# Performance work log

Measured on AMD Instinct MI355X. Metric: run time of the kernel, lower is better.

## Reference

```python
import jax, jax.numpy as jnp
import numpy as np

EPS_DENOM = 1e-7   # epsilon added to sigmoid-sum denominator in the torch code
EPS_NORM = 1e-5    # torch InstanceNorm1d default eps


def _fcnn(x, W1, b1, W2, b2):
    # FCNN: Linear -> ReLU -> Linear
    return jax.nn.relu(x @ W1 + b1) @ W2 + b2


def setup_inputs() -> dict:
    key = jax.random.key(0)
    N, E, D, H = 100000, 1600000, 32, 128  # nodes, edges, feature dim (c_in1=c_out2), hidden (c_out1)
    ks = jax.random.split(key, 11)
    node_features = jax.random.normal(ks[0], (N, D), jnp.float32)
    edge_features = jax.random.normal(ks[1], (E, D), jnp.float32)
    edge_index = jax.random.randint(ks[2], (2, E), 0, N, dtype=jnp.int64)
    sD = 1.0 / np.sqrt(D)
    sH = 1.0 / np.sqrt(H)
    # FCNN_one params
    W1a = jax.random.normal(ks[3], (D, H), jnp.float32) * sD
    b1a = jax.random.normal(ks[4], (H,), jnp.float32) * sD
    W2a = jax.random.normal(ks[5], (H, D), jnp.float32) * sH
    b2a = jax.random.normal(ks[6], (D,), jnp.float32) * sH
    # FCNN_two params
    W1b = jax.random.normal(ks[7], (D, H), jnp.float32) * sD
    b1b = jax.random.normal(ks[8], (H,), jnp.float32) * sD
    W2b = jax.random.normal(ks[9], (H, D), jnp.float32) * sH
    b2b = jax.random.normal(ks[10], (D,), jnp.float32) * sH
    return dict(node_features=node_features, edge_features=edge_features,
                W1a=W1a, b1a=b1a, W2a=W2a, b2a=b2a,
                W1b=W1b, b1b=b1b, W2b=W2b, b2b=b2b,
                edge_index=edge_index)


def reference(node_features, edge_features, W1a, b1a, W2a, b2a,
              W1b, b1b, W2b, b2b, edge_index):
    x = node_features                      # [N, D]
    N = x.shape[0]
    h1 = _fcnn(x, W1a, b1a, W2a, b2a)      # FCNN_one(x_i) for all nodes
    h2 = _fcnn(x, W1b, b1b, W2b, b2b)      # FCNN_two(x_j) for all nodes

    s = jax.nn.sigmoid(edge_features)      # [E, D]
    # node i gathers edges where it is src OR dst (both directions)
    seg = jnp.concatenate([edge_index[0], edge_index[1]])  # [2E] center node
    nbr = jnp.concatenate([edge_index[1], edge_index[0]])  # [2E] neighbor node
    s2 = jnp.concatenate([s, s], axis=0)                   # [2E, D]

    denom = EPS_DENOM + jax.ops.segment_sum(s2, seg, num_segments=N)  # [N, D]
    msg = (s2 / denom[seg]) * h2[nbr]                                 # [2E, D]
    agg = jax.ops.segment_sum(msg, seg, num_segments=N)               # [N, D]

    h = h1 + agg
    # InstanceNorm1d over the feature dim (no affine, biased variance); dropout is identity (eval)
    mu = jnp.mean(h, axis=-1, keepdims=True)
    var = jnp.var(h, axis=-1, keepdims=True)
    hn = (h - mu) * jax.lax.rsqrt(var + EPS_NORM)
    return x + jax.nn.relu(hn)
```

## Files before the change

### kernel.cpp

```cpp
#include <hip/hip_runtime.h>

#define EPS_DENOM 1e-7f
#define EPS_NORM  1e-5f

static constexpr int D  = 32;
static constexpr int H  = 128;
static constexpr int BK = 128;
static constexpr int CHUNK = 3072;
static constexpr int CAPMAX = 6144;

typedef _Float16 f16x8 __attribute__((ext_vector_type(8)));
typedef float    f32x4 __attribute__((ext_vector_type(4)));

__global__ __launch_bounds__(256) void fcnn_mfma_kernel(
    const float* __restrict__ x,
    const float* __restrict__ W1a, const float* __restrict__ b1a,
    const float* __restrict__ W2a, const float* __restrict__ b2a,
    const float* __restrict__ W1b, const float* __restrict__ b1b,
    const float* __restrict__ W2b, const float* __restrict__ b2b,
    float* __restrict__ h1, _Float16* __restrict__ h2h, int N)
{
    __shared__ _Float16 lds[30208];
    _Float16* xk = lds;

    const int tid = threadIdx.x;
    const int nb0 = blockIdx.x * 64;

    #pragma unroll
    for (int t = 0; t < 8; ++t) {
        int f = t * 256 + tid;
        int node = f >> 5, off = f & 31;
        int gn = nb0 + node;
        float v = (gn < N) ? x[(size_t)gn * 32 + off] : 0.0f;
        xk[node * 40 + off] = (_Float16)v;
    }
    for (int fc = 0; fc < 2; ++fc) {
        const float* W1 = fc ? W1b : W1a;
        const float* W2 = fc ? W2b : W2a;
        _Float16* w1t = lds + 2560 + fc * 5120;
        _Float16* w2t = lds + 12800 + fc * 4352;
        #pragma unroll
        for (int t = 0; t < 16; ++t) {
            int f = t * 256 + tid;
            w1t[(f & 127) * 40 + (f >> 7)] = (_Float16)W1[f];
        }
        #pragma unroll
        for (int t = 0; t < 16; ++t) {
            int f = t * 256 + tid;
            w2t[(f & 31) * 136 + (f >> 5)] = (_Float16)W2[f];
        }
    }
    __syncthreads();

    const int wid  = tid >> 6;
    const int lane = tid & 63;
    const int m    = lane & 15;
    const int g    = lane >> 4;
    _Float16* t1 = lds + 21504 + wid * 2176;

    f16x8 ax = *(const f16x8*)(xk + (wid * 16 + m) * 40 + g * 8);

    for (int fc = 0; fc < 2; ++fc) {
        const float* b1v = fc ? b1b : b1a;
        const float* b2v = fc ? b2b : b2a;
        const _Float16* w1t = lds + 2560 + fc * 5120;
        const _Float16* w2t = lds + 12800 + fc * 4352;

        for (int hb = 0; hb < 8; ++hb) {
            f16x8 bw = *(const f16x8*)(w1t + (hb * 16 + m) * 40 + g * 8);
            f32x4 c = {0.f, 0.f, 0.f, 0.f};
            c = __builtin_amdgcn_mfma_f32_16x16x32_f16(ax, bw, c, 0, 0, 0);
            float bias = b1v[hb * 16 + m];
            #pragma unroll
            for (int r = 0; r < 4; ++r) {
                float tv = fmaxf(c[r] + bias, 0.0f);
                t1[(g * 4 + r) * 136 + hb * 16 + m] = (_Float16)tv;
            }
        }

        for (int dt = 0; dt < 2; ++dt) {
            f32x4 c2 = {0.f, 0.f, 0.f, 0.f};
            #pragma unroll
            for (int kc = 0; kc < 4; ++kc) {
                f16x8 a2  = *(const f16x8*)(t1 + m * 136 + kc * 32 + g * 8);
                f16x8 b2w = *(const f16x8*)(w2t + (dt * 16 + m) * 136 + kc * 32 + g * 8);
                c2 = __builtin_amdgcn_mfma_f32_16x16x32_f16(a2, b2w, c2, 0, 0, 0);
            }
            float bias = b2v[dt * 16 + m];
            #pragma unroll
            for (int r = 0; r < 4; ++r) {
                int gn = nb0 + wid * 16 + g * 4 + r;
                if (gn < N) {
                    float val = c2[r] + bias;
                    if (fc == 0) h1[(size_t)gn * 32 + dt * 16 + m] = val;
                    else         h2h[(size_t)gn * 32 + dt * 16 + m] = (_Float16)val;
                }
            }
        }
        __syncthreads();
    }
}

__global__ __launch_bounds__(256) void sprep_kernel(
    const float* __restrict__ ef, unsigned char* __restrict__ sg8, int n4)
{
    int i = blockIdx.x * blockDim.x + threadIdx.x;
    if (i >= n4) return;
    float4 v = ((const float4*)ef)[i];
    uchar4 q;
    q.x = (unsigned char)(255.0f / (1.0f + __expf(-v.x)) + 0.5f);
    q.y = (unsigned char)(255.0f / (1.0f + __expf(-v.y)) + 0.5f);
    q.z = (unsigned char)(255.0f / (1.0f + __expf(-v.z)) + 0.5f);
    q.w = (unsigned char)(255.0f / (1.0f + __expf(-v.w)) + 0.5f);
    ((uchar4*)sg8)[i] = q;
}

__global__ __launch_bounds__(256) void bin1_kernel(
    const int* __restrict__ ei, int* __restrict__ gcursor,
    uint2* __restrict__ gadj, int E, int CAP)
{
    __shared__ uint2 recs[2 * CHUNK];
    __shared__ int cnt[1024];
    __shared__ int offs[1024];
    __shared__ int gbase[1024];
    __shared__ int partial[256];

    const int tid  = threadIdx.x;
    const int base = blockIdx.x * CHUNK;
    const int ne   = min(CHUNK, E - base);

    #pragma unroll
    for (int i = 0; i < 4; ++i) cnt[tid * 4 + i] = 0;
    __syncthreads();

    int av[CHUNK / 256], bv[CHUNK / 256];
    #pragma unroll
    for (int j = 0; j < CHUNK / 256; ++j) {
        int r = j * 256 + tid;
        if (r < ne) {
            int e = base + r;
            av[j] = ei[e]; bv[j] = ei[E + e];
            atomicAdd(&cnt[av[j] >> 7], 1);
            atomicAdd(&cnt[bv[j] >> 7], 1);
        } else av[j] = -1;
    }
    __syncthreads();

    int c0 = cnt[tid*4], c1 = cnt[tid*4+1], c2 = cnt[tid*4+2], c3 = cnt[tid*4+3];
    int psum = c0 + c1 + c2 + c3;
    partial[tid] = psum;
    __syncthreads();
    for (int off = 1; off < 256; off <<= 1) {
        int t = (tid >= off) ? partial[tid - off] : 0;
        __syncthreads();
        partial[tid] += t;
        __syncthreads();
    }
    int ex = partial[tid] - psum;
    offs[tid*4]   = ex;
    offs[tid*4+1] = ex + c0;
    offs[tid*4+2] = ex + c0 + c1;
    offs[tid*4+3] = ex + c0 + c1 + c2;
    cnt[tid*4]    = ex;
    cnt[tid*4+1]  = ex + c0;
    cnt[tid*4+2]  = ex + c0 + c1;
    cnt[tid*4+3]  = ex + c0 + c1 + c2;
    __syncthreads();

    #pragma unroll
    for (int j = 0; j < CHUNK / 256; ++j) {
        if (av[j] >= 0) {
            int e = base + j * 256 + tid;
            int a = av[j], b = bv[j];
            int pa = atomicAdd(&cnt[a >> 7], 1);
            recs[pa] = make_uint2(((unsigned)(a & 127) << 21) | (unsigned)e,
                                  ((unsigned)(a >> 7) << 17) | (unsigned)b);
            int pb = atomicAdd(&cnt[b >> 7], 1);
            recs[pb] = make_uint2(((unsigned)(b & 127) << 21) | (unsigned)e,
                                  ((unsigned)(b >> 7) << 17) | (unsigned)a);
        }
    }
    __syncthreads();

    #pragma unroll
    for (int i = 0; i < 4; ++i) {
        int bidx = tid * 4 + i;
        int c = cnt[bidx] - offs[bidx];
        if (c > 0) gbase[bidx] = atomicAdd(&gcursor[bidx], c);
    }
    __syncthreads();

    int total = 2 * ne;
    for (int i = tid; i < total; i += 256) {
        uint2 r = recs[i];
        int bidx = r.y >> 17;
        int dest = gbase[bidx] + (i - offs[bidx]);
        if (dest < CAP)
            gadj[(size_t)bidx * CAP + dest] = r;
    }
}

__global__ __launch_bounds__(256) void bin2_kernel(
    const int* __restrict__ gcursor, uint2* __restrict__ gadj,
    int* __restrict__ gstart, int* __restrict__ gdeg,
    int N, int CAP)
{
    __shared__ uint2 recs[CAPMAX];
    __shared__ int cnt[BK];
    __shared__ int sc[BK];
    __shared__ int lcur[BK];

    const int tid = threadIdx.x;
    const int bk  = blockIdx.x;
    const int count = min(gcursor[bk], CAP);
    uint2* seg = gadj + (size_t)bk * CAP;

    if (tid < BK) cnt[tid] = 0;
    for (int i = tid; i < count; i += 256) recs[i] = seg[i];
    __syncthreads();

    for (int i = tid; i < count; i += 256)
        atomicAdd(&cnt[(recs[i].x >> 21) & 127], 1);
    __syncthreads();

    int v = (tid < BK) ? cnt[tid] : 0;
    if (tid < BK) sc[tid] = v;
    __syncthreads();
    for (int off = 1; off < BK; off <<= 1) {
        int t = (tid < BK && tid >= off) ? sc[tid - off] : 0;
        __syncthreads();
        if (tid < BK) sc[tid] += t;
        __syncthreads();
    }
    if (tid < BK) {
        int excl = sc[tid] - v;
        lcur[tid] = excl;
        int gn = bk * BK + tid;
        if (gn < N) {
            gstart[gn] = bk * CAP + excl;
            gdeg[gn]   = v;
        }
    }
    __syncthreads();

    for (int i = tid; i < count; i += 256) {
        uint2 r = recs[i];
        int l = (r.x >> 21) & 127;
        int pos = atomicAdd(&lcur[l], 1);
        seg[pos] = make_uint2(r.x & 0x1FFFFFu, r.y & 0x1FFFFu);
    }
}

template <bool USE_SG>
__global__ __launch_bounds__(256) void gather_kernel(
    const float* __restrict__ x,  const unsigned char* __restrict__ sg8,
    const float* __restrict__ ef, const float* __restrict__ h1,
    const _Float16* __restrict__ h2h,
    const int* __restrict__ gstart, const int* __restrict__ gdeg,
    const uint2* __restrict__ adj2,
    float* __restrict__ out, int N)
{
    int t = blockIdx.x * blockDim.x + threadIdx.x;
    int n = t >> 5;
    int d = t & 31;
    if (n >= N) return;

    int start = gstart[n];
    int end   = start + gdeg[n];

    float s_sum = 0.0f, sh_sum = 0.0f;
    int k = start;
    for (; k + 4 <= end; k += 4) {
        uint2 r0 = adj2[k+0], r1 = adj2[k+1], r2 = adj2[k+2], r3 = adj2[k+3];
        float s0, s1, s2, s3;
        if (USE_SG) {
            s0 = (float)sg8[(size_t)r0.x * 32 + d] * (1.0f / 255.0f);
            s1 = (float)sg8[(size_t)r1.x * 32 + d] * (1.0f / 255.0f);
            s2 = (float)sg8[(size_t)r2.x * 32 + d] * (1.0f / 255.0f);
            s3 = (float)sg8[(size_t)r3.x * 32 + d] * (1.0f / 255.0f);
        } else {
            s0 = 1.0f / (1.0f + __expf(-ef[(size_t)r0.x * 32 + d]));
            s1 = 1.0f / (1.0f + __expf(-ef[(size_t)r1.x * 32 + d]));
            s2 = 1.0f / (1.0f + __expf(-ef[(size_t)r2.x * 32 + d]));
            s3 = 1.0f / (1.0f + __expf(-ef[(size_t)r3.x * 32 + d]));
        }
        float h0 = (float)h2h[(size_t)r0.y * 32 + d];
        float h1v = (float)h2h[(size_t)r1.y * 32 + d];
        float h2v = (float)h2h[(size_t)r2.y * 32 + d];
        float h3 = (float)h2h[(size_t)r3.y * 32 + d];
        s_sum += (s0 + s1) + (s2 + s3);
        sh_sum = fmaf(s0, h0, sh_sum);
        sh_sum = fmaf(s1, h1v, sh_sum);
        sh_sum = fmaf(s2, h2v, sh_sum);
        sh_sum = fmaf(s3, h3, sh_sum);
    }
    for (; k < end; ++k) {
        uint2 r = adj2[k];
        float s;
        if (USE_SG) s = (float)sg8[(size_t)r.x * 32 + d] * (1.0f / 255.0f);
        else        s = 1.0f / (1.0f + __expf(-ef[(size_t)r.x * 32 + d]));
        float hh = (float)h2h[(size_t)r.y * 32 + d];
        s_sum += s;
        sh_sum = fmaf(s, hh, sh_sum);
    }

    size_t idx = (size_t)n * 32 + d;
    float h = h1[idx] + sh_sum / (EPS_DENOM + s_sum);

    float sum = h, sq = h * h;
    #pragma unroll
    for (int off = 16; off > 0; off >>= 1) {
        sum += __shfl_xor(sum, off, 32);
        sq  += __shfl_xor(sq,  off, 32);
    }
    float mu  = sum * (1.0f / 32.0f);
    float var = fmaxf(sq * (1.0f / 32.0f) - mu * mu, 0.0f);
    float hn  = (h - mu) * rsqrtf(var + EPS_NORM);

    out[idx] = x[idx] + fmaxf(hn, 0.0f);
}

extern "C" void kernel_launch(void* const* d_in, const int* in_sizes, int n_in,
                              void* d_out, int out_size, void* d_ws, size_t ws_size,
                              hipStream_t stream)
{
    const float* x   = (const float*)d_in[0];
    const float* ef  = (const float*)d_in[1];
    const float* W1a = (const float*)d_in[2];
    const float* b1a = (const float*)d_in[3];
    const float* W2a = (const float*)d_in[4];
    const float* b2a = (const float*)d_in[5];
    const float* W1b = (const float*)d_in[6];
    const float* b1b = (const float*)d_in[7];
    const float* W2b = (const float*)d_in[8];
    const float* b2b = (const float*)d_in[9];
    const int*   ei  = (const int*)d_in[10];
    float* out = (float*)d_out;

    const int N  = in_sizes[0] / D;
    const int E  = in_sizes[1] / D;
    const int NB = (N + BK - 1) / BK;
    int CAP = (2 * E) / NB;
    CAP = CAP + CAP / 2;
    CAP = (CAP + 255) & ~255;
    if (CAP > CAPMAX) CAP = CAPMAX;

    char* p = (char*)d_ws;
    float*    h1      = (float*)p;    p += (size_t)N * 32 * 4;
    _Float16* h2h     = (_Float16*)p; p += (size_t)N * 32 * 2;
    int*      gcursor = (int*)p;      p += 1024 * 4;
    int*      gstart  = (int*)p;      p += (size_t)N * 4;
    int*      gdeg    = (int*)p;      p += (size_t)N * 4;
    p = (char*)(((uintptr_t)p + 31) & ~(uintptr_t)31);
    uint2*    gadj    = (uint2*)p;    p += (size_t)NB * CAP * 8;
    p = (char*)(((uintptr_t)p + 31) & ~(uintptr_t)31);
    unsigned char* sg8 = (unsigned char*)p;
    const bool use_sg = ((size_t)(p - (char*)d_ws) + (size_t)E * 32) <= ws_size;

    hipMemsetAsync(gcursor, 0, 1024 * 4, stream);

    fcnn_mfma_kernel<<<(N + 63) / 64, 256, 0, stream>>>(
        x, W1a, b1a, W2a, b2a, W1b, b1b, W2b, b2b, h1, h2h, N);

    if (use_sg) {
        int n4 = E * 8;
        sprep_kernel<<<(n4 + 255) / 256, 256, 0, stream>>>(ef, sg8, n4);
    }

    bin1_kernel<<<(E + CHUNK - 1) / CHUNK, 256, 0, stream>>>(ei, gcursor, gadj, E, CAP);
    bin2_kernel<<<NB, 256, 0, stream>>>(gcursor, gadj, gstart, gdeg, N, CAP);

    int gthreads = N * 32;
    if (use_sg)
        gather_kernel<true><<<(gthreads + 255) / 256, 256, 0, stream>>>(
            x, sg8, ef, h1, h2h, gstart, gdeg, gadj, out, N);
    else
        gather_kernel<false><<<(gthreads + 255) / 256, 256, 0, stream>>>(
            x, sg8, ef, h1, h2h, gstart, gdeg, gadj, out, N);
}
```

Baseline: 547.6 us.

## Fuse FCNN, sigmoid quantization and binning pass into one heterogeneous launch

Merges the FCNN MFMA kernel, the sigmoid-to-uint8 prep kernel and the first binning pass into a single kernel. Blocks are divided into stripes of 8 slots: 3 FCNN tiles, 4 grid-stride sigmoid workers and 1 binning chunk, so the independent stages overlap across CUs instead of running back to back. bin2 is also widened to 512 threads. The cost is a larger shared-memory footprint for every block, which can limit occupancy, plus some block-role imbalance.

```diff
diff --git a/kernel.cpp b/kernel.cpp
--- a/kernel.cpp
+++ b/kernel.cpp
@@ -12,195 +12,232 @@
 typedef _Float16 f16x8 __attribute__((ext_vector_type(8)));
 typedef float    f32x4 __attribute__((ext_vector_type(4)));
 
-__global__ __launch_bounds__(256) void fcnn_mfma_kernel(
+__global__ __launch_bounds__(256) void prep_kernel(
     const float* __restrict__ x,
     const float* __restrict__ W1a, const float* __restrict__ b1a,
     const float* __restrict__ W2a, const float* __restrict__ b2a,
     const float* __restrict__ W1b, const float* __restrict__ b1b,
     const float* __restrict__ W2b, const float* __restrict__ b2b,
-    float* __restrict__ h1, _Float16* __restrict__ h2h, int N)
+    float* __restrict__ h1, _Float16* __restrict__ h2h,
+    const float* __restrict__ ef, unsigned char* __restrict__ sg8,
+    const int* __restrict__ ei, int* __restrict__ gcursor,
+    uint2* __restrict__ gadj,
+    int N, int E, int CAP, int F, int B, int stripes, int n4, int do_sg)
 {
-    __shared__ _Float16 lds[30208];
-    _Float16* xk = lds;
-
-    const int tid = threadIdx.x;
-    const int nb0 = blockIdx.x * 64;
-
-    #pragma unroll
-    for (int t = 0; t < 8; ++t) {
-        int f = t * 256 + tid;
-        int node = f >> 5, off = f & 31;
-        int gn = nb0 + node;
-        float v = (gn < N) ? x[(size_t)gn * 32 + off] : 0.0f;
-        xk[node * 40 + off] = (_Float16)v;
-    }
-    for (int fc = 0; fc < 2; ++fc) {
-        const float* W1 = fc ? W1b : W1a;
-        const float* W2 = fc ? W2b : W2a;
-        _Float16* w1t = lds + 2560 + fc * 5120;
-        _Float16* w2t = lds + 12800 + fc * 4352;
+    __shared__ unsigned long long smem_u64[7808];
+
+    const int tid    = threadIdx.x;
+    const int stripe = blockIdx.x >> 3;
+    const int slot   = blockIdx.x & 7;
+
+    if (slot < 3) {
+        const int fid = stripe * 3 + slot;
+        if (fid >= F) return;
+        _Float16* lds = (_Float16*)smem_u64;
+        _Float16* xk  = lds;
+        const int nb0 = fid * 64;
+
         #pragma unroll
-        for (int t = 0; t < 16; ++t) {
+        for (int t = 0; t < 8; ++t) {
             int f = t * 256 + tid;
-            w1t[(f & 127) * 40 + (f >> 7)] = (_Float16)W1[f];
-        }
-        #pragma unroll
-        for (int t = 0; t < 16; ++t) {
-            int f = t * 256 + tid;
-            w2t[(f & 31) * 136 + (f >> 5)] = (_Float16)W2[f];
-        }
-    }
-    __syncthreads();
-
-    const int wid  = tid >> 6;
-    const int lane = tid & 63;
-    const int m    = lane & 15;
-    const int g    = lane >> 4;
-    _Float16* t1 = lds + 21504 + wid * 2176;
-
-    f16x8 ax = *(const f16x8*)(xk + (wid * 16 + m) * 40 + g * 8);
-
-    for (int fc = 0; fc < 2; ++fc) {
-        const float* b1v = fc ? b1b : b1a;
-        const float* b2v = fc ? b2b : b2a;
-        const _Float16* w1t = lds + 2560 + fc * 5120;
-        const _Float16* w2t = lds + 12800 + fc * 4352;
-
-        for (int hb = 0; hb < 8; ++hb) {
-            f16x8 bw = *(const f16x8*)(w1t + (hb * 16 + m) * 40 + g * 8);
-            f32x4 c = {0.f, 0.f, 0.f, 0.f};
-            c = __builtin_amdgcn_mfma_f32_16x16x32_f16(ax, bw, c, 0, 0, 0);
-            float bias = b1v[hb * 16 + m];
+            int node = f >> 5, off = f & 31;
+            int gn = nb0 + node;
+            float v = (gn < N) ? x[(size_t)gn * 32 + off] : 0.0f;
+            xk[node * 40 + off] = (_Float16)v;
+        }
+        for (int fc = 0; fc < 2; ++fc) {
+            const float* W1 = fc ? W1b : W1a;
+            const float* W2 = fc ? W2b : W2a;
+            _Float16* w1t = lds + 2560 + fc * 5120;
+            _Float16* w2t = lds + 12800 + fc * 4352;
             #pragma unroll
-            for (int r = 0; r < 4; ++r) {
-                float tv = fmaxf(c[r] + bias, 0.0f);
-                t1[(g * 4 + r) * 136 + hb * 16 + m] = (_Float16)tv;
+            for (int t = 0; t < 16; ++t) {
+                int f = t * 256 + tid;
+                w1t[(f & 127) * 40 + (f >> 7)] = (_Float16)W1[f];
             }
-        }
-
-        for (int dt = 0; dt < 2; ++dt) {
-            f32x4 c2 = {0.f, 0.f, 0.f, 0.f};
             #pragma unroll
-            for (int kc = 0; kc < 4; ++kc) {
-                f16x8 a2  = *(const f16x8*)(t1 + m * 136 + kc * 32 + g * 8);
-                f16x8 b2w = *(const f16x8*)(w2t + (dt * 16 + m) * 136 + kc * 32 + g * 8);
-                c2 = __builtin_amdgcn_mfma_f32_16x16x32_f16(a2, b2w, c2, 0, 0, 0);
+            for (int t = 0; t < 16; ++t) {
+                int f = t * 256 + tid;
+                w2t[(f & 31) * 136 + (f >> 5)] = (_Float16)W2[f];
             }
-            float bias = b2v[dt * 16 + m];
-            #pragma unroll
-            for (int r = 0; r < 4; ++r) {
-                int gn = nb0 + wid * 16 + g * 4 + r;
-                if (gn < N) {
-                    float val = c2[r] + bias;
-                    if (fc == 0) h1[(size_t)gn * 32 + dt * 16 + m] = val;
-                    else         h2h[(size_t)gn * 32 + dt * 16 + m] = (_Float16)val;
+        }
+        __syncthreads();
+
+        const int wid  = tid >> 6;
+        const int lane = tid & 63;
+        const int m    = lane & 15;
+        const int g    = lane >> 4;
+        _Float16* t1 = lds + 21504 + wid * 2176;
+
+        f16x8 ax = *(const f16x8*)(xk + (wid * 16 + m) * 40 + g * 8);
+
+        for (int fc = 0; fc < 2; ++fc) {
+            const float* b1v = fc ? b1b : b1a;
+            const float* b2v = fc ? b2b : b2a;
+            const _Float16* w1t = lds + 2560 + fc * 5120;
+            const _Float16* w2t = lds + 12800 + fc * 4352;
+
+            for (int hb = 0; hb < 8; ++hb) {
+                f16x8 bw = *(const f16x8*)(w1t + (hb * 16 + m) * 40 + g * 8);
+                f32x4 c = {0.f, 0.f, 0.f, 0.f};
+                c = __builtin_amdgcn_mfma_f32_16x16x32_f16(ax, bw, c, 0, 0, 0);
+                float bias = b1v[hb * 16 + m];
+                #pragma unroll
+                for (int r = 0; r < 4; ++r) {
+                    float tv = fmaxf(c[r] + bias, 0.0f);
+                    t1[(g * 4 + r) * 136 + hb * 16 + m] = (_Float16)tv;
                 }
             }
-        }
-        __syncthreads();
+
+            for (int dt = 0; dt < 2; ++dt) {
+                f32x4 c2 = {0.f, 0.f, 0.f, 0.f};
+                #pragma unroll
+                for (int kc = 0; kc < 4; ++kc) {
+                    f16x8 a2  = *(const f16x8*)(t1 + m * 136 + kc * 32 + g * 8);
+                    f16x8 b2w = *(const f16x8*)(w2t + (dt * 16 + m) * 136 + kc * 32 + g * 8);
+                    c2 = __builtin_amdgcn_mfma_f32_16x16x32_f16(a2, b2w, c2, 0, 0, 0);
+                }
+                float bias = b2v[dt * 16 + m];
+                #pragma unroll
+                for (int r = 0; r < 4; ++r) {
+                    int gn = nb0 + wid * 16 + g * 4 + r;
+                    if (gn < N) {
+                        float val = c2[r] + bias;
+                        if (fc == 0) h1[(size_t)gn * 32 + dt * 16 + m] = val;
+                        else         h2h[(size_t)gn * 32 + dt * 16 + m] = (_Float16)val;
+                    }
+                }
+            }
+            __syncthreads();
+        }
+    } else if (slot < 7) {
+        if (!do_sg) return;
+        const int sid  = stripe * 4 + (slot - 3);
+        const int nthr = stripes * 4 * 256;
+        const float4* efc = (const float4*)ef;
+        uchar4* sq = (uchar4*)sg8;
+        int i = sid * 256 + tid;
+        for (; i + 3 * nthr < n4; i += 4 * nthr) {
+            float4 v0 = efc[i];
+            float4 v1 = efc[i + nthr];
+            float4 v2 = efc[i + 2 * nthr];
+            float4 v3 = efc[i + 3 * nthr];
+            uchar4 q0, q1, q2, q3;
+            q0.x = (unsigned char)(255.0f / (1.0f + __expf(-v0.x)) + 0.5f);
+            q0.y = (unsigned char)(255.0f / (1.0f + __expf(-v0.y)) + 0.5f);
+            q0.z = (unsigned char)(255.0f / (1.0f + __expf(-v0.z)) + 0.5f);
+            q0.w = (unsigned char)(255.0f / (1.0f + __expf(-v0.w)) + 0.5f);
+            q1.x = (unsigned char)(255.0f / (1.0f + __expf(-v1.x)) + 0.5f);
+            q1.y = (unsigned char)(255.0f / (1.0f + __expf(-v1.y)) + 0.5f);
+            q1.z = (unsigned char)(255.0f / (1.0f + __expf(-v1.z)) + 0.5f);
+            q1.w = (unsigned char)(255.0f / (1.0f + __expf(-v1.w)) + 0.5f);
+            q2.x = (unsigned char)(255.0f / (1.0f + __expf(-v2.x)) + 0.5f);
+            q2.y = (unsigned char)(255.0f / (1.0f + __expf(-v2.y)) + 0.5f);
+            q2.z = (unsigned char)(255.0f / (1.0f + __expf(-v2.z)) + 0.5f);
+            q2.w = (unsigned char)(255.0f / (1.0f + __expf(-v2.w)) + 0.5f);
+            q3.x = (unsigned char)(255.0f / (1.0f + __expf(-v3.x)) + 0.5f);
+            q3.y = (unsigned char)(255.0f / (1.0f + __expf(-v3.y)) + 0.5f);
+            q3.z = (unsigned char)(255.0f / (1.0f + __expf(-v3.z)) + 0.5f);
+            q3.w = (unsigned char)(255.0f / (1.0f + __expf(-v3.w)) + 0.5f);
+            sq[i]            = q0;
+            sq[i + nthr]     = q1;
+            sq[i + 2 * nthr] = q2;
+            sq[i + 3 * nthr] = q3;
+        }
+        for (; i < n4; i += nthr) {
+            float4 v = efc[i];
+            uchar4 q;
+            q.x = (unsigned char)(255.0f / (1.0f + __expf(-v.x)) + 0.5f);
+            q.y = (unsigned char)(255.0f / (1.0f + __expf(-v.y)) + 0.5f);
+            q.z = (unsigned char)(255.0f / (1.0f + __expf(-v.z)) + 0.5f);
+            q.w = (unsigned char)(255.0f / (1.0f + __expf(-v.w)) + 0.5f);
+            sq[i] = q;
+        }
+    } else {
+        const int bid = stripe;
+        if (bid >= B) return;
+        uint2* recs  = (uint2*)smem_u64;
+        int* cnt     = (int*)((char*)smem_u64 + 49152);
+        int* offs    = (int*)((char*)smem_u64 + 53248);
+        int* gbase   = (int*)((char*)smem_u64 + 57344);
+        int* partial = (int*)((char*)smem_u64 + 61440);
+
+        const int base = bid * CHUNK;
+        const int ne   = min(CHUNK, E - base);
+
+        #pragma unroll
+        for (int i = 0; i < 4; ++i) cnt[tid * 4 + i] = 0;
+        __syncthreads();
+
+        int av[CHUNK / 256], bv[CHUNK / 256];
+        #pragma unroll
+        for (int j = 0; j < CHUNK / 256; ++j) {
+            int r = j * 256 + tid;
+            if (r < ne) {
+                int e = base + r;
+                av[j] = ei[e]; bv[j] = ei[E + e];
+                atomicAdd(&cnt[av[j] >> 7], 1);
+                atomicAdd(&cnt[bv[j] >> 7], 1);
+            } else av[j] = -1;
+        }
+        __syncthreads();
+
+        int c0 = cnt[tid*4], c1 = cnt[tid*4+1], c2 = cnt[tid*4+2], c3 = cnt[tid*4+3];
+        int psum = c0 + c1 + c2 + c3;
+        partial[tid] = psum;
+        __syncthreads();
+        for (int off = 1; off < 256; off <<= 1) {
+            int t = (tid >= off) ? partial[tid - off] : 0;
+            __syncthreads();
+            partial[tid] += t;
+            __syncthreads();
+        }
+        int ex = partial[tid] - psum;
+        offs[tid*4]   = ex;
+        offs[tid*4+1] = ex + c0;
+        offs[tid*4+2] = ex + c0 + c1;
+        offs[tid*4+3] = ex + c0 + c1 + c2;
+        cnt[tid*4]    = ex;
+        cnt[tid*4+1]  = ex + c0;
+        cnt[tid*4+2]  = ex + c0 + c1;
+        cnt[tid*4+3]  = ex + c0 + c1 + c2;
+        __syncthreads();
+
+        #pragma unroll
+        for (int j = 0; j < CHUNK / 256; ++j) {
+            if (av[j] >= 0) {
+                int e = base + j * 256 + tid;
+                int a = av[j], b = bv[j];
+                int pa = atomicAdd(&cnt[a >> 7], 1);
+                recs[pa] = make_uint2(((unsigned)(a & 127) << 21) | (unsigned)e,
+                                      ((unsigned)(a >> 7) << 17) | (unsigned)b);
+                int pb = atomicAdd(&cnt[b >> 7], 1);
+                recs[pb] = make_uint2(((unsigned)(b & 127) << 21) | (unsigned)e,
+                                      ((unsigned)(b >> 7) << 17) | (unsigned)a);
+            }
+        }
+        __syncthreads();
+
+        #pragma unroll
+        for (int i = 0; i < 4; ++i) {
+            int bidx = tid * 4 + i;
+            int c = cnt[bidx] - offs[bidx];
+            if (c > 0) gbase[bidx] = atomicAdd(&gcursor[bidx], c);
+        }
+        __syncthreads();
+
+        int total = 2 * ne;
+        for (int i = tid; i < total; i += 256) {
+            uint2 r = recs[i];
+            int bidx = r.y >> 17;
+            int dest = gbase[bidx] + (i - offs[bidx]);
+            if (dest < CAP)
+                gadj[(size_t)bidx * CAP + dest] = r;
+        }
     }
 }
 
-__global__ __launch_bounds__(256) void sprep_kernel(
-    const float* __restrict__ ef, unsigned char* __restrict__ sg8, int n4)
-{
-    int i = blockIdx.x * blockDim.x + threadIdx.x;
-    if (i >= n4) return;
-    float4 v = ((const float4*)ef)[i];
-    uchar4 q;
-    q.x = (unsigned char)(255.0f / (1.0f + __expf(-v.x)) + 0.5f);
-    q.y = (unsigned char)(255.0f / (1.0f + __expf(-v.y)) + 0.5f);
-    q.z = (unsigned char)(255.0f / (1.0f + __expf(-v.z)) + 0.5f);
-    q.w = (unsigned char)(255.0f / (1.0f + __expf(-v.w)) + 0.5f);
-    ((uchar4*)sg8)[i] = q;
-}
-
-__global__ __launch_bounds__(256) void bin1_kernel(
-    const int* __restrict__ ei, int* __restrict__ gcursor,
-    uint2* __restrict__ gadj, int E, int CAP)
-{
-    __shared__ uint2 recs[2 * CHUNK];
-    __shared__ int cnt[1024];
-    __shared__ int offs[1024];
-    __shared__ int gbase[1024];
-    __shared__ int partial[256];
-
-    const int tid  = threadIdx.x;
-    const int base = blockIdx.x * CHUNK;
-    const int ne   = min(CHUNK, E - base);
-
-    #pragma unroll
-    for (int i = 0; i < 4; ++i) cnt[tid * 4 + i] = 0;
-    __syncthreads();
-
-    int av[CHUNK / 256], bv[CHUNK / 256];
-    #pragma unroll
-    for (int j = 0; j < CHUNK / 256; ++j) {
-        int r = j * 256 + tid;
-        if (r < ne) {
-            int e = base + r;
-            av[j] = ei[e]; bv[j] = ei[E + e];
-            atomicAdd(&cnt[av[j] >> 7], 1);
-            atomicAdd(&cnt[bv[j] >> 7], 1);
-        } else av[j] = -1;
-    }
-    __syncthreads();
-
-    int c0 = cnt[tid*4], c1 = cnt[tid*4+1], c2 = cnt[tid*4+2], c3 = cnt[tid*4+3];
-    int psum = c0 + c1 + c2 + c3;
-    partial[tid] = psum;
-    __syncthreads();
-    for (int off = 1; off < 256; off <<= 1) {
-        int t = (tid >= off) ? partial[tid - off] : 0;
-        __syncthreads();
-        partial[tid] += t;
-        __syncthreads();
-    }
-    int ex = partial[tid] - psum;
-    offs[tid*4]   = ex;
-    offs[tid*4+1] = ex + c0;
-    offs[tid*4+2] = ex + c0 + c1;
-    offs[tid*4+3] = ex + c0 + c1 + c2;
-    cnt[tid*4]    = ex;
-    cnt[tid*4+1]  = ex + c0;
-    cnt[tid*4+2]  = ex + c0 + c1;
-    cnt[tid*4+3]  = ex + c0 + c1 + c2;
-    __syncthreads();
-
-    #pragma unroll
-    for (int j = 0; j < CHUNK / 256; ++j) {
-        if (av[j] >= 0) {
-            int e = base + j * 256 + tid;
-            int a = av[j], b = bv[j];
-            int pa = atomicAdd(&cnt[a >> 7], 1);
-            recs[pa] = make_uint2(((unsigned)(a & 127) << 21) | (unsigned)e,
-                                  ((unsigned)(a >> 7) << 17) | (unsigned)b);
-            int pb = atomicAdd(&cnt[b >> 7], 1);
-            recs[pb] = make_uint2(((unsigned)(b & 127) << 21) | (unsigned)e,
-                                  ((unsigned)(b >> 7) << 17) | (unsigned)a);
-        }
-    }
-    __syncthreads();
-
-    #pragma unroll
-    for (int i = 0; i < 4; ++i) {
-        int bidx = tid * 4 + i;
-        int c = cnt[bidx] - offs[bidx];
-        if (c > 0) gbase[bidx] = atomicAdd(&gcursor[bidx], c);
-    }
-    __syncthreads();
-
-    int total = 2 * ne;
-    for (int i = tid; i < total; i += 256) {
-        uint2 r = recs[i];
-        int bidx = r.y >> 17;
-        int dest = gbase[bidx] + (i - offs[bidx]);
-        if (dest < CAP)
-            gadj[(size_t)bidx * CAP + dest] = r;
-    }
-}
-
-__global__ __launch_bounds__(256) void bin2_kernel(
+__global__ __launch_bounds__(512) void bin2_kernel(
     const int* __restrict__ gcursor, uint2* __restrict__ gadj,
     int* __restrict__ gstart, int* __restrict__ gdeg,
     int N, int CAP)
@@ -216,10 +253,10 @@
     uint2* seg = gadj + (size_t)bk * CAP;
 
     if (tid < BK) cnt[tid] = 0;
-    for (int i = tid; i < count; i += 256) recs[i] = seg[i];
+    for (int i = tid; i < count; i += 512) recs[i] = seg[i];
     __syncthreads();
 
-    for (int i = tid; i < count; i += 256)
+    for (int i = tid; i < count; i += 512)
         atomicAdd(&cnt[(recs[i].x >> 21) & 127], 1);
     __syncthreads();
 
@@ -243,7 +280,7 @@
     }
     __syncthreads();
 
-    for (int i = tid; i < count; i += 256) {
+    for (int i = tid; i < count; i += 512) {
         uint2 r = recs[i];
         int l = (r.x >> 21) & 127;
         int pos = atomicAdd(&lcur[l], 1);
@@ -359,16 +396,18 @@
 
     hipMemsetAsync(gcursor, 0, 1024 * 4, stream);
 
-    fcnn_mfma_kernel<<<(N + 63) / 64, 256, 0, stream>>>(
-        x, W1a, b1a, W2a, b2a, W1b, b1b, W2b, b2b, h1, h2h, N);
-
-    if (use_sg) {
-        int n4 = E * 8;
-        sprep_kernel<<<(n4 + 255) / 256, 256, 0, stream>>>(ef, sg8, n4);
-    }
-
-    bin1_kernel<<<(E + CHUNK - 1) / CHUNK, 256, 0, stream>>>(ei, gcursor, gadj, E, CAP);
-    bin2_kernel<<<NB, 256, 0, stream>>>(gcursor, gadj, gstart, gdeg, N, CAP);
+    const int F = (N + 63) / 64;
+    const int B = (E + CHUNK - 1) / CHUNK;
+    int stripes = (F + 2) / 3;
+    if (B > stripes) stripes = B;
+    const int n4 = E * 8;
+
+    prep_kernel<<<stripes * 8, 256, 0, stream>>>(
+        x, W1a, b1a, W2a, b2a, W1b, b1b, W2b, b2b, h1, h2h,
+        ef, sg8, ei, gcursor, gadj,
+        N, E, CAP, F, B, stripes, n4, use_sg ? 1 : 0);
+
+    bin2_kernel<<<NB, 512, 0, stream>>>(gcursor, gadj, gstart, gdeg, N, CAP);
 
     int gthreads = N * 32;
     if (use_sg)
```

Measured after the change: 539.0 us. About the same (-1.6%).

## Fuse FCNN and edge-binning into one interleaved kernel, widen bin2, unroll gather

Applied to the files above, without the earlier changes.

Merges the MFMA FCNN kernel and the first edge-binning pass into a single launch, with block slots interleaved 3:1 so compute-bound FCNN blocks and memory/atomic-bound binning blocks run concurrently on the GPU. The two roles share one LDS buffer sized for the larger of the two. bin2 now runs 512 threads per block, and the gather loop gains an 8-way unrolled path for more loads in flight. The shared LDS footprint and the heterogeneous blocks may reduce occupancy for the FCNN part.

```diff
diff --git a/kernel.cpp b/kernel.cpp
--- a/kernel.cpp
+++ b/kernel.cpp
@@ -12,92 +12,184 @@
 typedef _Float16 f16x8 __attribute__((ext_vector_type(8)));
 typedef float    f32x4 __attribute__((ext_vector_type(4)));
 
-__global__ __launch_bounds__(256) void fcnn_mfma_kernel(
+__global__ __launch_bounds__(256) void fb_kernel(
     const float* __restrict__ x,
     const float* __restrict__ W1a, const float* __restrict__ b1a,
     const float* __restrict__ W2a, const float* __restrict__ b2a,
     const float* __restrict__ W1b, const float* __restrict__ b1b,
     const float* __restrict__ W2b, const float* __restrict__ b2b,
-    float* __restrict__ h1, _Float16* __restrict__ h2h, int N)
+    float* __restrict__ h1, _Float16* __restrict__ h2h,
+    const int* __restrict__ ei, int* __restrict__ gcursor,
+    uint2* __restrict__ gadj,
+    int N, int E, int CAP, int F, int B)
 {
-    __shared__ _Float16 lds[30208];
-    _Float16* xk = lds;
-
-    const int tid = threadIdx.x;
-    const int nb0 = blockIdx.x * 64;
-
-    #pragma unroll
-    for (int t = 0; t < 8; ++t) {
-        int f = t * 256 + tid;
-        int node = f >> 5, off = f & 31;
-        int gn = nb0 + node;
-        float v = (gn < N) ? x[(size_t)gn * 32 + off] : 0.0f;
-        xk[node * 40 + off] = (_Float16)v;
-    }
-    for (int fc = 0; fc < 2; ++fc) {
-        const float* W1 = fc ? W1b : W1a;
-        const float* W2 = fc ? W2b : W2a;
-        _Float16* w1t = lds + 2560 + fc * 5120;
-        _Float16* w2t = lds + 12800 + fc * 4352;
+    __shared__ unsigned long long smem_u64[7808];
+
+    const int tid    = threadIdx.x;
+    const int stripe = blockIdx.x >> 2;
+    const int slot   = blockIdx.x & 3;
+
+    if (slot < 3) {
+        const int fid = stripe * 3 + slot;
+        if (fid >= F) return;
+        _Float16* lds = (_Float16*)smem_u64;
+        _Float16* xk  = lds;
+        const int nb0 = fid * 64;
+
         #pragma unroll
-        for (int t = 0; t < 16; ++t) {
+        for (int t = 0; t < 8; ++t) {
             int f = t * 256 + tid;
-            w1t[(f & 127) * 40 + (f >> 7)] = (_Float16)W1[f];
-        }
-        #pragma unroll
-        for (int t = 0; t < 16; ++t) {
-            int f = t * 256 + tid;
-            w2t[(f & 31) * 136 + (f >> 5)] = (_Float16)W2[f];
-        }
-    }
-    __syncthreads();
-
-    const int wid  = tid >> 6;
-    const int lane = tid & 63;
-    const int m    = lane & 15;
-    const int g    = lane >> 4;
-    _Float16* t1 = lds + 21504 + wid * 2176;
-
-    f16x8 ax = *(const f16x8*)(xk + (wid * 16 + m) * 40 + g * 8);
-
-    for (int fc = 0; fc < 2; ++fc) {
-        const float* b1v = fc ? b1b : b1a;
-        const float* b2v = fc ? b2b : b2a;
-        const _Float16* w1t = lds + 2560 + fc * 5120;
-        const _Float16* w2t = lds + 12800 + fc * 4352;
-
-        for (int hb = 0; hb < 8; ++hb) {
-            f16x8 bw = *(const f16x8*)(w1t + (hb * 16 + m) * 40 + g * 8);
-            f32x4 c = {0.f, 0.f, 0.f, 0.f};
-            c = __builtin_amdgcn_mfma_f32_16x16x32_f16(ax, bw, c, 0, 0, 0);
-            float bias = b1v[hb * 16 + m];
+            int node = f >> 5, off = f & 31;
+            int gn = nb0 + node;
+            float v = (gn < N) ? x[(size_t)gn * 32 + off] : 0.0f;
+            xk[node * 40 + off] = (_Float16)v;
+        }
+        for (int fc = 0; fc < 2; ++fc) {
+            const float* W1 = fc ? W1b : W1a;
+            const float* W2 = fc ? W2b : W2a;
+            _Float16* w1t = lds + 2560 + fc * 5120;
+            _Float16* w2t = lds + 12800 + fc * 4352;
             #pragma unroll
-            for (int r = 0; r < 4; ++r) {
-                float tv = fmaxf(c[r] + bias, 0.0f);
-                t1[(g * 4 + r) * 136 + hb * 16 + m] = (_Float16)tv;
+            for (int t = 0; t < 16; ++t) {
+                int f = t * 256 + tid;
+                w1t[(f & 127) * 40 + (f >> 7)] = (_Float16)W1[f];
             }
-        }
-
-        for (int dt = 0; dt < 2; ++dt) {
-            f32x4 c2 = {0.f, 0.f, 0.f, 0.f};
             #pragma unroll
-            for (int kc = 0; kc < 4; ++kc) {
-                f16x8 a2  = *(const f16x8*)(t1 + m * 136 + kc * 32 + g * 8);
-                f16x8 b2w = *(const f16x8*)(w2t + (dt * 16 + m) * 136 + kc * 32 + g * 8);
-                c2 = __builtin_amdgcn_mfma_f32_16x16x32_f16(a2, b2w, c2, 0, 0, 0);
+            for (int t = 0; t < 16; ++t) {
+                int f = t * 256 + tid;
+                w2t[(f & 31) * 136 + (f >> 5)] = (_Float16)W2[f];
             }
-            float bias = b2v[dt * 16 + m];
-            #pragma unroll
-            for (int r = 0; r < 4; ++r) {
-                int gn = nb0 + wid * 16 + g * 4 + r;
-                if (gn < N) {
-                    float val = c2[r] + bias;
-                    if (fc == 0) h1[(size_t)gn * 32 + dt * 16 + m] = val;
-                    else         h2h[(size_t)gn * 32 + dt * 16 + m] = (_Float16)val;
+        }
+        __syncthreads();
+
+        const int wid  = tid >> 6;
+        const int lane = tid & 63;
+        const int m    = lane & 15;
+        const int g    = lane >> 4;
+        _Float16* t1 = lds + 21504 + wid * 2176;
+
+        f16x8 ax = *(const f16x8*)(xk + (wid * 16 + m) * 40 + g * 8);
+
+        for (int fc = 0; fc < 2; ++fc) {
+            const float* b1v = fc ? b1b : b1a;
+            const float* b2v = fc ? b2b : b2a;
+            const _Float16* w1t = lds + 2560 + fc * 5120;
+            const _Float16* w2t = lds + 12800 + fc * 4352;
+
+            for (int hb = 0; hb < 8; ++hb) {
+                f16x8 bw = *(const f16x8*)(w1t + (hb * 16 + m) * 40 + g * 8);
+                f32x4 c = {0.f, 0.f, 0.f, 0.f};
+                c = __builtin_amdgcn_mfma_f32_16x16x32_f16(ax, bw, c, 0, 0, 0);
+                float bias = b1v[hb * 16 + m];
+                #pragma unroll
+                for (int r = 0; r < 4; ++r) {
+                    float tv = fmaxf(c[r] + bias, 0.0f);
+                    t1[(g * 4 + r) * 136 + hb * 16 + m] = (_Float16)tv;
                 }
             }
-        }
-        __syncthreads();
+
+            for (int dt = 0; dt < 2; ++dt) {
+                f32x4 c2 = {0.f, 0.f, 0.f, 0.f};
+                #pragma unroll
+                for (int kc = 0; kc < 4; ++kc) {
+                    f16x8 a2  = *(const f16x8*)(t1 + m * 136 + kc * 32 + g * 8);
+                    f16x8 b2w = *(const f16x8*)(w2t + (dt * 16 + m) * 136 + kc * 32 + g * 8);
+                    c2 = __builtin_amdgcn_mfma_f32_16x16x32_f16(a2, b2w, c2, 0, 0, 0);
+                }
+                float bias = b2v[dt * 16 + m];
+                #pragma unroll
+                for (int r = 0; r < 4; ++r) {
+                    int gn = nb0 + wid * 16 + g * 4 + r;
+                    if (gn < N) {
+                        float val = c2[r] + bias;
+                        if (fc == 0) h1[(size_t)gn * 32 + dt * 16 + m] = val;
+                        else         h2h[(size_t)gn * 32 + dt * 16 + m] = (_Float16)val;
+                    }
+                }
+            }
+            __syncthreads();
+        }
+    } else {
+        const int bid = stripe;
+        if (bid >= B) return;
+        uint2* recs  = (uint2*)smem_u64;
+        int* cnt     = (int*)((char*)smem_u64 + 49152);
+        int* offs    = (int*)((char*)smem_u64 + 53248);
+        int* gbase   = (int*)((char*)smem_u64 + 57344);
+        int* partial = (int*)((char*)smem_u64 + 61440);
+
+        const int base = bid * CHUNK;
+        const int ne   = min(CHUNK, E - base);
+
+        #pragma unroll
+        for (int i = 0; i < 4; ++i) cnt[tid * 4 + i] = 0;
+        __syncthreads();
+
+        int av[CHUNK / 256], bv[CHUNK / 256];
+        #pragma unroll
+        for (int j = 0; j < CHUNK / 256; ++j) {
+            int r = j * 256 + tid;
+            if (r < ne) {
+                int e = base + r;
+                av[j] = ei[e]; bv[j] = ei[E + e];
+                atomicAdd(&cnt[av[j] >> 7], 1);
+                atomicAdd(&cnt[bv[j] >> 7], 1);
+            } else av[j] = -1;
+        }
+        __syncthreads();
+
+        int c0 = cnt[tid*4], c1 = cnt[tid*4+1], c2 = cnt[tid*4+2], c3 = cnt[tid*4+3];
+        int psum = c0 + c1 + c2 + c3;
+        partial[tid] = psum;
+        __syncthreads();
+        for (int off = 1; off < 256; off <<= 1) {
+            int t = (tid >= off) ? partial[tid - off] : 0;
+            __syncthreads();
+            partial[tid] += t;
+            __syncthreads();
+        }
+        int ex = partial[tid] - psum;
+        offs[tid*4]   = ex;
+        offs[tid*4+1] = ex + c0;
+        offs[tid*4+2] = ex + c0 + c1;
+        offs[tid*4+3] = ex + c0 + c1 + c2;
+        cnt[tid*4]    = ex;
+        cnt[tid*4+1]  = ex + c0;
+        cnt[tid*4+2]  = ex + c0 + c1;
+        cnt[tid*4+3]  = ex + c0 + c1 + c2;
+        __syncthreads();
+
+        #pragma unroll
+        for (int j = 0; j < CHUNK / 256; ++j) {
+            if (av[j] >= 0) {
+                int e = base + j * 256 + tid;
+                int a = av[j], b = bv[j];
+                int pa = atomicAdd(&cnt[a >> 7], 1);
+                recs[pa] = make_uint2(((unsigned)(a & 127) << 21) | (unsigned)e,
+                                      ((unsigned)(a >> 7) << 17) | (unsigned)b);
+                int pb = atomicAdd(&cnt[b >> 7], 1);
+                recs[pb] = make_uint2(((unsigned)(b & 127) << 21) | (unsigned)e,
+                                      ((unsigned)(b >> 7) << 17) | (unsigned)a);
+            }
+        }
+        __syncthreads();
+
+        #pragma unroll
+        for (int i = 0; i < 4; ++i) {
+            int bidx = tid * 4 + i;
+            int c = cnt[bidx] - offs[bidx];
+            if (c > 0) gbase[bidx] = atomicAdd(&gcursor[bidx], c);
+        }
+        __syncthreads();
+
+        int total = 2 * ne;
+        for (int i = tid; i < total; i += 256) {
+            uint2 r = recs[i];
+            int bidx = r.y >> 17;
+            int dest = gbase[bidx] + (i - offs[bidx]);
+            if (dest < CAP)
+                gadj[(size_t)bidx * CAP + dest] = r;
+        }
     }
 }
 
@@ -115,92 +207,7 @@
     ((uchar4*)sg8)[i] = q;
 }
 
-__global__ __launch_bounds__(256) void bin1_kernel(
-    const int* __restrict__ ei, int* __restrict__ gcursor,
-    uint2* __restrict__ gadj, int E, int CAP)
-{
-    __shared__ uint2 recs[2 * CHUNK];
-    __shared__ int cnt[1024];
-    __shared__ int offs[1024];
-    __shared__ int gbase[1024];
-    __shared__ int partial[256];
-
-    const int tid  = threadIdx.x;
-    const int base = blockIdx.x * CHUNK;
-    const int ne   = min(CHUNK, E - base);
-
-    #pragma unroll
-    for (int i = 0; i < 4; ++i) cnt[tid * 4 + i] = 0;
-    __syncthreads();
-
-    int av[CHUNK / 256], bv[CHUNK / 256];
-    #pragma unroll
-    for (int j = 0; j < CHUNK / 256; ++j) {
-        int r = j * 256 + tid;
-        if (r < ne) {
-            int e = base + r;
-            av[j] = ei[e]; bv[j] = ei[E + e];
-            atomicAdd(&cnt[av[j] >> 7], 1);
-            atomicAdd(&cnt[bv[j] >> 7], 1);
-        } else av[j] = -1;
-    }
-    __syncthreads();
-
-    int c0 = cnt[tid*4], c1 = cnt[tid*4+1], c2 = cnt[tid*4+2], c3 = cnt[tid*4+3];
-    int psum = c0 + c1 + c2 + c3;
-    partial[tid] = psum;
-    __syncthreads();
-    for (int off = 1; off < 256; off <<= 1) {
-        int t = (tid >= off) ? partial[tid - off] : 0;
-        __syncthreads();
-        partial[tid] += t;
-        __syncthreads();
-    }
-    int ex = partial[tid] - psum;
-    offs[tid*4]   = ex;
-    offs[tid*4+1] = ex + c0;
-    offs[tid*4+2] = ex + c0 + c1;
-    offs[tid*4+3] = ex + c0 + c1 + c2;
-    cnt[tid*4]    = ex;
-    cnt[tid*4+1]  = ex + c0;
-    cnt[tid*4+2]  = ex + c0 + c1;
-    cnt[tid*4+3]  = ex + c0 + c1 + c2;
-    __syncthreads();
-
-    #pragma unroll
-    for (int j = 0; j < CHUNK / 256; ++j) {
-        if (av[j] >= 0) {
-            int e = base + j * 256 + tid;
-            int a = av[j], b = bv[j];
-            int pa = atomicAdd(&cnt[a >> 7], 1);
-            recs[pa] = make_uint2(((unsigned)(a & 127) << 21) | (unsigned)e,
-                                  ((unsigned)(a >> 7) << 17) | (unsigned)b);
-            int pb = atomicAdd(&cnt[b >> 7], 1);
-            recs[pb] = make_uint2(((unsigned)(b & 127) << 21) | (unsigned)e,
-                                  ((unsigned)(b >> 7) << 17) | (unsigned)a);
-        }
-    }
-    __syncthreads();
-
-    #pragma unroll
-    for (int i = 0; i < 4; ++i) {
-        int bidx = tid * 4 + i;
-        int c = cnt[bidx] - offs[bidx];
-        if (c > 0) gbase[bidx] = atomicAdd(&gcursor[bidx], c);
-    }
-    __syncthreads();
-
-    int total = 2 * ne;
-    for (int i = tid; i < total; i += 256) {
-        uint2 r = recs[i];
-        int bidx = r.y >> 17;
-        int dest = gbase[bidx] + (i - offs[bidx]);
-        if (dest < CAP)
-            gadj[(size_t)bidx * CAP + dest] = r;
-    }
-}
-
-__global__ __launch_bounds__(256) void bin2_kernel(
+__global__ __launch_bounds__(512) void bin2_kernel(
     const int* __restrict__ gcursor, uint2* __restrict__ gadj,
     int* __restrict__ gstart, int* __restrict__ gdeg,
     int N, int CAP)
@@ -216,10 +223,10 @@
     uint2* seg = gadj + (size_t)bk * CAP;
 
     if (tid < BK) cnt[tid] = 0;
-    for (int i = tid; i < count; i += 256) recs[i] = seg[i];
+    for (int i = tid; i < count; i += 512) recs[i] = seg[i];
     __syncthreads();
 
-    for (int i = tid; i < count; i += 256)
+    for (int i = tid; i < count; i += 512)
         atomicAdd(&cnt[(recs[i].x >> 21) & 127], 1);
     __syncthreads();
 
@@ -243,7 +250,7 @@
     }
     __syncthreads();
 
-    for (int i = tid; i < count; i += 256) {
+    for (int i = tid; i < count; i += 512) {
         uint2 r = recs[i];
         int l = (r.x >> 21) & 127;
         int pos = atomicAdd(&lcur[l], 1);
@@ -270,6 +277,47 @@
 
     float s_sum = 0.0f, sh_sum = 0.0f;
     int k = start;
+    for (; k + 8 <= end; k += 8) {
+        uint2 r0 = adj2[k+0], r1 = adj2[k+1], r2 = adj2[k+2], r3 = adj2[k+3];
+        uint2 r4 = adj2[k+4], r5 = adj2[k+5], r6 = adj2[k+6], r7 = adj2[k+7];
+        float s0, s1, s2, s3, s4, s5, s6, s7;
+        if (USE_SG) {
+            s0 = (float)sg8[(size_t)r0.x * 32 + d] * (1.0f / 255.0f);
+            s1 = (float)sg8[(size_t)r1.x * 32 + d] * (1.0f / 255.0f);
+            s2 = (float)sg8[(size_t)r2.x * 32 + d] * (1.0f / 255.0f);
+            s3 = (float)sg8[(size_t)r3.x * 32 + d] * (1.0f / 255.0f);
+            s4 = (float)sg8[(size_t)r4.x * 32 + d] * (1.0f / 255.0f);
+            s5 = (float)sg8[(size_t)r5.x * 32 + d] * (1.0f / 255.0f);
+            s6 = (float)sg8[(size_t)r6.x * 32 + d] * (1.0f / 255.0f);
+            s7 = (float)sg8[(size_t)r7.x * 32 + d] * (1.0f / 255.0f);
+        } else {
+            s0 = 1.0f / (1.0f + __expf(-ef[(size_t)r0.x * 32 + d]));
+            s1 = 1.0f / (1.0f + __expf(-ef[(size_t)r1.x * 32 + d]));
+            s2 = 1.0f / (1.0f + __expf(-ef[(size_t)r2.x * 32 + d]));
+            s3 = 1.0f / (1.0f + __expf(-ef[(size_t)r3.x * 32 + d]));
+            s4 = 1.0f / (1.0f + __expf(-ef[(size_t)r4.x * 32 + d]));
+            s5 = 1.0f / (1.0f + __expf(-ef[(size_t)r5.x * 32 + d]));
+            s6 = 1.0f / (1.0f + __expf(-ef[(size_t)r6.x * 32 + d]));
+            s7 = 1.0f / (1.0f + __expf(-ef[(size_t)r7.x * 32 + d]));
+        }
+        float h0 = (float)h2h[(size_t)r0.y * 32 + d];
+        float h1v = (float)h2h[(size_t)r1.y * 32 + d];
+        float h2v = (float)h2h[(size_t)r2.y * 32 + d];
+        float h3 = (float)h2h[(size_t)r3.y * 32 + d];
+        float h4 = (float)h2h[(size_t)r4.y * 32 + d];
+        float h5 = (float)h2h[(size_t)r5.y * 32 + d];
+        float h6 = (float)h2h[(size_t)r6.y * 32 + d];
+        float h7 = (float)h2h[(size_t)r7.y * 32 + d];
+        s_sum += ((s0 + s1) + (s2 + s3)) + ((s4 + s5) + (s6 + s7));
+        sh_sum = fmaf(s0, h0, sh_sum);
+        sh_sum = fmaf(s1, h1v, sh_sum);
+        sh_sum = fmaf(s2, h2v, sh_sum);
+        sh_sum = fmaf(s3, h3, sh_sum);
+        sh_sum = fmaf(s4, h4, sh_sum);
+        sh_sum = fmaf(s5, h5, sh_sum);
+        sh_sum = fmaf(s6, h6, sh_sum);
+        sh_sum = fmaf(s7, h7, sh_sum);
+    }
     for (; k + 4 <= end; k += 4) {
         uint2 r0 = adj2[k+0], r1 = adj2[k+1], r2 = adj2[k+2], r3 = adj2[k+3];
         float s0, s1, s2, s3;
@@ -359,16 +407,21 @@
 
     hipMemsetAsync(gcursor, 0, 1024 * 4, stream);
 
-    fcnn_mfma_kernel<<<(N + 63) / 64, 256, 0, stream>>>(
-        x, W1a, b1a, W2a, b2a, W1b, b1b, W2b, b2b, h1, h2h, N);
+    const int F = (N + 63) / 64;
+    const int B = (E + CHUNK - 1) / CHUNK;
+    int stripes = (F + 2) / 3;
+    if (B > stripes) stripes = B;
 
     if (use_sg) {
         int n4 = E * 8;
         sprep_kernel<<<(n4 + 255) / 256, 256, 0, stream>>>(ef, sg8, n4);
     }
 
-    bin1_kernel<<<(E + CHUNK - 1) / CHUNK, 256, 0, stream>>>(ei, gcursor, gadj, E, CAP);
-    bin2_kernel<<<NB, 256, 0, stream>>>(gcursor, gadj, gstart, gdeg, N, CAP);
+    fb_kernel<<<stripes * 4, 256, 0, stream>>>(
+        x, W1a, b1a, W2a, b2a, W1b, b1b, W2b, b2b, h1, h2h,
+        ei, gcursor, gadj, N, E, CAP, F, B);
+
+    bin2_kernel<<<NB, 512, 0, stream>>>(gcursor, gadj, gstart, gdeg, N, CAP);
 
     int gthreads = N * 32;
     if (use_sg)
```

After: 531.6 us. 1.03x faster.
